# Kernel optimization log

Measured on AMD Instinct MI355X. Metric: run time of the kernel, lower is better.

## Reference

```python
import jax, jax.numpy as jnp
import numpy as np

N, K, F = 262144, 256, 128
LAMB = 1.0
EPS = 1e-16


def setup_inputs() -> dict:
    key = jax.random.key(0)
    kx, = jax.random.split(key, 1)
    x = jax.random.normal(kx, (N, F), dtype=jnp.float32)
    # Faithful SVD-orthonormal init of cluster centers (num_clusters > feature_size branch)
    rng = np.random.RandomState(0)
    m_np = rng.rand(K, F)
    m_np = m_np.T                      # (F, K) since K > F
    _, _, vh = np.linalg.svd(m_np, full_matrices=False)  # vh: (F, K)
    m_np = vh[:K].T                    # (K, F), orthonormal columns
    m = jnp.asarray(m_np, dtype=jnp.float32)
    s1 = jnp.ones((K,), dtype=jnp.float32)
    s2 = jnp.ones((K,), dtype=jnp.float32)
    return {"x": x, "m": m, "s1": s1, "s2": s2}


def _p_all(x, m, s):
    # x: (N,F), m: (K,F), s: (K,) -> p: (N,K)
    # squared distances via gram expansion (single GEMM instead of per-sample loop)
    d2 = (jnp.sum(x * x, axis=1, keepdims=True)
          + jnp.sum(m * m, axis=1)[None, :]
          - 2.0 * (x @ m.T))
    d2 = jnp.maximum(d2, 0.0)
    logits = -d2 / (s * s)[None, :]
    return jax.nn.softmax(logits, axis=-1)


def _entropy(p):
    # shannon entropy with the original's clamping of p into (0,1)
    p = jnp.clip(p, EPS, 1.0 - EPS)
    return -jnp.sum(p * jnp.log(p), axis=-1)


def reference(x, m, s1, s2):
    # F.normalize(x): L2-normalize rows with eps=1e-12
    xn = x / jnp.maximum(jnp.linalg.norm(x, axis=1, keepdims=True), 1e-12)
    p = _p_all(xn, m, s1)              # (N,K)
    intra = jnp.mean(_entropy(p))      # scalar
    # inter: entropy of the assignment of the mean center against all centers
    xm = jnp.mean(m, axis=0)           # (F,)
    d = jnp.linalg.norm(xm[None, :] - m, axis=1)  # (K,)
    pi = jax.nn.softmax(-((d / s2) ** 2))
    inter = _entropy(pi)
    total = intra - LAMB * inter
    return (total, intra, inter)
```

## Files before the change

kernel.cpp:

```cpp
#include <hip/hip_runtime.h>
#include <hip/hip_bf16.h>


#define N_ROWS 262144

typedef __attribute__((ext_vector_type(8))) short bf16x8;
typedef __attribute__((ext_vector_type(4))) float f32x4;
typedef __attribute__((ext_vector_type(4))) unsigned short u16x4;

__device__ __forceinline__ unsigned short bf16_rne(float x) {
    unsigned int u = __float_as_uint(x);
    u += 0x7FFFu + ((u >> 16) & 1u);
    return (unsigned short)(u >> 16);
}
__device__ __forceinline__ float bf16f(unsigned short h) {
    return __uint_as_float(((unsigned int)h) << 16);
}

__global__ __launch_bounds__(256) void prep(
    const float* __restrict__ m, const float* __restrict__ s1,
    unsigned short* __restrict__ mhi_g, float* __restrict__ mn2_g,
    float* __restrict__ invs_g)
{
    const int t    = threadIdx.x;
    const int lane = t & 63;
    const int k    = blockIdx.x * 8 + (t >> 5);
    const int f4   = t & 31;
    float4 v = reinterpret_cast<const float4*>(m)[k * 32 + f4];
    float pn = v.x*v.x + v.y*v.y + v.z*v.z + v.w*v.w;
    #pragma unroll
    for (int msk = 1; msk <= 16; msk <<= 1) pn += __shfl_xor(pn, msk);
    if ((lane & 31) == 0) {
        mn2_g[k] = pn;
        float sv = s1[k];
        invs_g[k] = 1.0f / (sv * sv);
    }
    const int f0 = f4 << 2;
    const int c = k >> 4, n = k & 15, s = f0 >> 5, blk = (f0 >> 3) & 3, i0 = f0 & 7;
    const int elem = ((c * 4 + s) * 64 + blk * 16 + n) * 8 + i0;
    float xs[4] = {v.x, v.y, v.z, v.w};
    u16x4 hh;
    #pragma unroll
    for (int q = 0; q < 4; ++q) hh[q] = bf16_rne(xs[q]);
    *(u16x4*)(mhi_g + elem) = hh;
}

__global__ __launch_bounds__(512, 4) void fused_main(
    const float* __restrict__ x, const unsigned short* __restrict__ mhi_g,
    const float* __restrict__ mn2_g, const float* __restrict__ invs_g,
    float* __restrict__ blocksum)
{
    extern __shared__ char smem[];
    unsigned short* mhi = (unsigned short*)smem;
    float* mn2  = (float*)(smem + 65536);
    float* invs = (float*)(smem + 65536 + 1024);
    float* entw = (float*)(smem + 65536 + 2048);

    const int tid  = threadIdx.x;
    const int lane = tid & 63;
    const int w    = tid >> 6;
    const int rw   = lane & 15;
    const int blkl = lane >> 4;

    {
        const uint4* s4 = (const uint4*)mhi_g;
        uint4* d4 = (uint4*)mhi;
        #pragma unroll
        for (int it = 0; it < 8; ++it) d4[tid + it * 512] = s4[tid + it * 512];
        if (tid < 256) { mn2[tid] = mn2_g[tid]; invs[tid] = invs_g[tid]; }
    }
    __syncthreads();

    const int rbase = blockIdx.x * 128 + w * 16;
    const float* xrow = x + (size_t)(rbase + rw) * 128 + blkl * 8;

    f32x4 acc[16];
    #pragma unroll
    for (int c = 0; c < 16; ++c) acc[c] = f32x4{0.f, 0.f, 0.f, 0.f};

    float n2 = 0.0f;
    float4 u = *(const float4*)(xrow);
    float4 v = *(const float4*)(xrow + 4);

    #pragma unroll
    for (int s = 0; s < 4; ++s) {
        bf16x8 ahi, alo;
        {
            float xs[8] = {u.x, u.y, u.z, u.w, v.x, v.y, v.z, v.w};
            #pragma unroll
            for (int q = 0; q < 8; ++q) {
                n2 += xs[q] * xs[q];
                unsigned short h = bf16_rne(xs[q]);
                float r = xs[q] - bf16f(h);
                ahi[q] = (short)h;
                alo[q] = (short)bf16_rne(r);
            }
        }
        if (s < 3) {
            u = *(const float4*)(xrow + (s + 1) * 32);
            v = *(const float4*)(xrow + (s + 1) * 32 + 4);
        }
        #pragma unroll
        for (int c = 0; c < 16; ++c) {
            bf16x8 bh = *(const bf16x8*)(mhi + ((c * 4 + s) * 64 + lane) * 8);
            acc[c] = __builtin_amdgcn_mfma_f32_16x16x32_bf16(alo, bh, acc[c], 0, 0, 0);
            acc[c] = __builtin_amdgcn_mfma_f32_16x16x32_bf16(ahi, bh, acc[c], 0, 0, 0);
        }
    }

    n2 += __shfl_xor(n2, 16);
    n2 += __shfl_xor(n2, 32);
    float a2 = 2.0f / fmaxf(sqrtf(n2), 1e-12f);
    float arow[4];
    #pragma unroll
    for (int reg = 0; reg < 4; ++reg)
        arow[reg] = __shfl(a2, blkl * 4 + reg);

    float bkv[16], isv[16];
    #pragma unroll
    for (int c = 0; c < 16; ++c) {
        int col = c * 16 + rw;
        bkv[c] = 1.0f + mn2[col];
        isv[c] = invs[col];
    }

    float ent = 0.0f;
    #pragma unroll
    for (int reg = 0; reg < 4; ++reg) {
        float S = 0.f, T = 0.f;
        #pragma unroll
        for (int c = 0; c < 16; ++c) {
            float l = fminf(arow[reg] * acc[c][reg] - bkv[c], 0.0f) * isv[c];
            float e = __expf(l);
            S += e;
            T += l * e;
        }
        #pragma unroll
        for (int msk = 1; msk <= 8; msk <<= 1) {
            S += __shfl_xor(S, msk);
            T += __shfl_xor(T, msk);
        }
        if (rw == 0) ent += __logf(S) - T / S;
    }
    ent += __shfl_xor(ent, 16);
    ent += __shfl_xor(ent, 32);
    if (lane == 0) entw[w] = ent;
    __syncthreads();
    if (tid == 0) {
        float b = 0.f;
        #pragma unroll
        for (int i = 0; i < 8; ++i) b += entw[i];
        blocksum[blockIdx.x] = b;
    }
}

__global__ __launch_bounds__(256) void finalize(
    const float* __restrict__ blocksum, const float* __restrict__ m,
    const float* __restrict__ s2, float* __restrict__ out)
{
    __shared__ float xmp[256];
    __shared__ float xm[128];
    __shared__ double dred[4];
    __shared__ float redM[4], redS[4], redT[4];
    const int tid = threadIdx.x;
    const int lane = tid & 63;
    const int w = tid >> 6;

    double ds = 0.0;
    #pragma unroll
    for (int j = 0; j < 8; ++j) ds += (double)blocksum[tid + 256 * j];
    #pragma unroll
    for (int msk = 1; msk <= 32; msk <<= 1) ds += __shfl_xor(ds, msk);
    if (lane == 0) dred[w] = ds;

    {
        const int f = tid & 127, half = tid >> 7;
        const float* mp = m + (size_t)half * 128 * 128 + f;
        float cs = 0.f;
        #pragma unroll 8
        for (int k = 0; k < 128; ++k) cs += mp[(size_t)k * 128];
        xmp[tid] = cs;
    }
    __syncthreads();
    if (tid < 128) xm[tid] = (xmp[tid] + xmp[tid + 128]) * (1.0f / 256.0f);
    __syncthreads();

    float d2 = 0.f;
    {
        const float4* mr = (const float4*)(m + (size_t)tid * 128);
        const float4* xv4 = (const float4*)xm;
        #pragma unroll 8
        for (int j = 0; j < 32; ++j) {
            float4 mv = mr[j], xv = xv4[j];
            float dx = xv.x - mv.x, dy = xv.y - mv.y,
                  dz = xv.z - mv.z, dw = xv.w - mv.w;
            d2 += dx*dx + dy*dy + dz*dz + dw*dw;
        }
    }
    float dd = sqrtf(d2);
    float r = dd / s2[tid];
    float lg = -(r * r);

    float mx = lg;
    #pragma unroll
    for (int msk = 1; msk <= 32; msk <<= 1) mx = fmaxf(mx, __shfl_xor(mx, msk));
    if (lane == 0) redM[w] = mx;
    __syncthreads();
    float bmx = fmaxf(fmaxf(redM[0], redM[1]), fmaxf(redM[2], redM[3]));
    float d = lg - bmx;
    float e = __expf(d);
    float S = e, T = d * e;
    #pragma unroll
    for (int msk = 1; msk <= 32; msk <<= 1) {
        S += __shfl_xor(S, msk);
        T += __shfl_xor(T, msk);
    }
    if (lane == 0) { redS[w] = S; redT[w] = T; }
    __syncthreads();
    if (tid == 0) {
        float Sa = redS[0] + redS[1] + redS[2] + redS[3];
        float Ta = redT[0] + redT[1] + redT[2] + redT[3];
        float inter = __logf(Sa) - Ta / Sa;
        double intra_d = dred[0] + dred[1] + dred[2] + dred[3];
        float intra = (float)(intra_d / (double)N_ROWS);
        out[0] = intra - inter;
        out[1] = intra;
        out[2] = inter;
    }
}

extern "C" void kernel_launch(void* const* d_in, const int* in_sizes, int n_in,
                              void* d_out, int out_size, void* d_ws, size_t ws_size,
                              hipStream_t stream) {
    const float* x  = (const float*)d_in[0];
    const float* m  = (const float*)d_in[1];
    const float* s1 = (const float*)d_in[2];
    const float* s2 = (const float*)d_in[3];
    float* out = (float*)d_out;

    char* ws = (char*)d_ws;
    unsigned short* mhi_g = (unsigned short*)ws;
    float* mn2_g  = (float*)(ws + 65536);
    float* invs_g = (float*)(ws + 65536 + 1024);
    float* blocksum = (float*)(ws + 65536 + 2048);

    const size_t shbytes = 65536 + 2048 + 32;
    static bool attr_set = false;
    if (!attr_set) {
        (void)hipFuncSetAttribute((const void*)fused_main,
                                  hipFuncAttributeMaxDynamicSharedMemorySize,
                                  (int)shbytes);
        attr_set = true;
    }

    prep<<<dim3(32), dim3(256), 0, stream>>>(m, s1, mhi_g, mn2_g, invs_g);
    fused_main<<<dim3(2048), dim3(512), shbytes, stream>>>(x, mhi_g, mn2_g, invs_g, blocksum);
    finalize<<<dim3(1), dim3(256), 0, stream>>>(blocksum, m, s2, out);
}
```

Baseline: 225.9 us.

## Hold centroid matrix in registers and loop each wave over many row tiles

The main kernel now runs as a persistent-style grid of 256 blocks. Each wave keeps the whole bf16 centroid matrix in registers (64 bf16x8 vectors) and processes 16 tiles of 16 rows, prefetching the next tile's x while computing the current one. This removes the per-block LDS copy of the centroids, the per-fragment LDS reads and the block-level sync. The cost is very high register pressure at one block of 256 threads per CU, so there is little occupancy left to hide latency. The finalize kernel is widened to 1024 threads, drops its max-reduction, and sums per-wave partials.

```diff
diff --git a/kernel.cpp b/kernel.cpp
--- a/kernel.cpp
+++ b/kernel.cpp
@@ -45,171 +45,158 @@
     *(u16x4*)(mhi_g + elem) = hh;
 }
 
-__global__ __launch_bounds__(512, 4) void fused_main(
+__global__ __launch_bounds__(256, 1) void fused_main(
     const float* __restrict__ x, const unsigned short* __restrict__ mhi_g,
     const float* __restrict__ mn2_g, const float* __restrict__ invs_g,
-    float* __restrict__ blocksum)
+    float* __restrict__ wavesum)
 {
-    extern __shared__ char smem[];
-    unsigned short* mhi = (unsigned short*)smem;
-    float* mn2  = (float*)(smem + 65536);
-    float* invs = (float*)(smem + 65536 + 1024);
-    float* entw = (float*)(smem + 65536 + 2048);
-
     const int tid  = threadIdx.x;
     const int lane = tid & 63;
     const int w    = tid >> 6;
     const int rw   = lane & 15;
     const int blkl = lane >> 4;
-
-    {
-        const uint4* s4 = (const uint4*)mhi_g;
-        uint4* d4 = (uint4*)mhi;
-        #pragma unroll
-        for (int it = 0; it < 8; ++it) d4[tid + it * 512] = s4[tid + it * 512];
-        if (tid < 256) { mn2[tid] = mn2_g[tid]; invs[tid] = invs_g[tid]; }
-    }
-    __syncthreads();
-
-    const int rbase = blockIdx.x * 128 + w * 16;
-    const float* xrow = x + (size_t)(rbase + rw) * 128 + blkl * 8;
-
-    f32x4 acc[16];
-    #pragma unroll
-    for (int c = 0; c < 16; ++c) acc[c] = f32x4{0.f, 0.f, 0.f, 0.f};
-
-    float n2 = 0.0f;
-    float4 u = *(const float4*)(xrow);
-    float4 v = *(const float4*)(xrow + 4);
-
+    const int gw   = blockIdx.x * 4 + w;
+
+    bf16x8 B[64];
+    #pragma unroll
+    for (int j = 0; j < 64; ++j)
+        B[j] = *(const bf16x8*)(mhi_g + (j * 64 + lane) * 8);
+
+    float bkv[16], isv[16];
+    #pragma unroll
+    for (int c = 0; c < 16; ++c) {
+        bkv[c] = 1.0f + mn2_g[c * 16 + rw];
+        isv[c] = invs_g[c * 16 + rw];
+    }
+
+    const float* xbase = x + (size_t)(gw * 256 + rw) * 128 + blkl * 8;
+
+    float4 px[8];
     #pragma unroll
     for (int s = 0; s < 4; ++s) {
-        bf16x8 ahi, alo;
-        {
-            float xs[8] = {u.x, u.y, u.z, u.w, v.x, v.y, v.z, v.w};
+        px[2*s]   = *(const float4*)(xbase + s * 32);
+        px[2*s+1] = *(const float4*)(xbase + s * 32 + 4);
+    }
+
+    float ent = 0.0f;
+
+    for (int t = 0; t < 16; ++t) {
+        bf16x8 ah[4], al[4];
+        float n2 = 0.0f;
+        #pragma unroll
+        for (int s = 0; s < 4; ++s) {
+            float xs[8] = {px[2*s].x, px[2*s].y, px[2*s].z, px[2*s].w,
+                           px[2*s+1].x, px[2*s+1].y, px[2*s+1].z, px[2*s+1].w};
             #pragma unroll
             for (int q = 0; q < 8; ++q) {
                 n2 += xs[q] * xs[q];
                 unsigned short h = bf16_rne(xs[q]);
                 float r = xs[q] - bf16f(h);
-                ahi[q] = (short)h;
-                alo[q] = (short)bf16_rne(r);
-            }
-        }
-        if (s < 3) {
-            u = *(const float4*)(xrow + (s + 1) * 32);
-            v = *(const float4*)(xrow + (s + 1) * 32 + 4);
-        }
-        #pragma unroll
-        for (int c = 0; c < 16; ++c) {
-            bf16x8 bh = *(const bf16x8*)(mhi + ((c * 4 + s) * 64 + lane) * 8);
-            acc[c] = __builtin_amdgcn_mfma_f32_16x16x32_bf16(alo, bh, acc[c], 0, 0, 0);
-            acc[c] = __builtin_amdgcn_mfma_f32_16x16x32_bf16(ahi, bh, acc[c], 0, 0, 0);
-        }
-    }
-
-    n2 += __shfl_xor(n2, 16);
-    n2 += __shfl_xor(n2, 32);
-    float a2 = 2.0f / fmaxf(sqrtf(n2), 1e-12f);
-    float arow[4];
-    #pragma unroll
-    for (int reg = 0; reg < 4; ++reg)
-        arow[reg] = __shfl(a2, blkl * 4 + reg);
-
-    float bkv[16], isv[16];
-    #pragma unroll
-    for (int c = 0; c < 16; ++c) {
-        int col = c * 16 + rw;
-        bkv[c] = 1.0f + mn2[col];
-        isv[c] = invs[col];
-    }
-
-    float ent = 0.0f;
-    #pragma unroll
-    for (int reg = 0; reg < 4; ++reg) {
-        float S = 0.f, T = 0.f;
-        #pragma unroll
-        for (int c = 0; c < 16; ++c) {
-            float l = fminf(arow[reg] * acc[c][reg] - bkv[c], 0.0f) * isv[c];
-            float e = __expf(l);
-            S += e;
-            T += l * e;
-        }
-        #pragma unroll
-        for (int msk = 1; msk <= 8; msk <<= 1) {
-            S += __shfl_xor(S, msk);
-            T += __shfl_xor(T, msk);
-        }
-        if (rw == 0) ent += __logf(S) - T / S;
-    }
+                ah[s][q] = (short)h;
+                al[s][q] = (short)bf16_rne(r);
+            }
+        }
+        if (t != 15) {
+            const float* p = xbase + (size_t)(t + 1) * 16 * 128;
+            #pragma unroll
+            for (int s = 0; s < 4; ++s) {
+                px[2*s]   = *(const float4*)(p + s * 32);
+                px[2*s+1] = *(const float4*)(p + s * 32 + 4);
+            }
+        }
+        f32x4 acc[16];
+        #pragma unroll
+        for (int c = 0; c < 16; ++c) acc[c] = f32x4{0.f, 0.f, 0.f, 0.f};
+        #pragma unroll
+        for (int s = 0; s < 4; ++s) {
+            #pragma unroll
+            for (int c = 0; c < 16; ++c) {
+                acc[c] = __builtin_amdgcn_mfma_f32_16x16x32_bf16(al[s], B[c*4+s], acc[c], 0, 0, 0);
+                acc[c] = __builtin_amdgcn_mfma_f32_16x16x32_bf16(ah[s], B[c*4+s], acc[c], 0, 0, 0);
+            }
+        }
+        n2 += __shfl_xor(n2, 16);
+        n2 += __shfl_xor(n2, 32);
+        float a2 = 2.0f / fmaxf(sqrtf(n2), 1e-12f);
+        #pragma unroll
+        for (int reg = 0; reg < 4; ++reg) {
+            float ar = __shfl(a2, blkl * 4 + reg);
+            float S = 0.f, T = 0.f;
+            #pragma unroll
+            for (int c = 0; c < 16; ++c) {
+                float l = fminf(ar * acc[c][reg] - bkv[c], 0.0f) * isv[c];
+                float e = __expf(l);
+                S += e;
+                T += l * e;
+            }
+            #pragma unroll
+            for (int msk = 1; msk <= 8; msk <<= 1) {
+                S += __shfl_xor(S, msk);
+                T += __shfl_xor(T, msk);
+            }
+            if (rw == 0) ent += __logf(S) - T / S;
+        }
+    }
+
     ent += __shfl_xor(ent, 16);
     ent += __shfl_xor(ent, 32);
-    if (lane == 0) entw[w] = ent;
-    __syncthreads();
-    if (tid == 0) {
-        float b = 0.f;
-        #pragma unroll
-        for (int i = 0; i < 8; ++i) b += entw[i];
-        blocksum[blockIdx.x] = b;
-    }
-}
-
-__global__ __launch_bounds__(256) void finalize(
-    const float* __restrict__ blocksum, const float* __restrict__ m,
+    if (lane == 0) wavesum[gw] = ent;
+}
+
+__global__ __launch_bounds__(1024) void finalize(
+    const float* __restrict__ wavesum, const float* __restrict__ m,
     const float* __restrict__ s2, float* __restrict__ out)
 {
-    __shared__ float xmp[256];
+    __shared__ float xmp[8][128];
     __shared__ float xm[128];
-    __shared__ double dred[4];
-    __shared__ float redM[4], redS[4], redT[4];
-    const int tid = threadIdx.x;
+    __shared__ double dred[16];
+    __shared__ float redS[16], redT[16];
+    const int tid  = threadIdx.x;
     const int lane = tid & 63;
-    const int w = tid >> 6;
-
-    double ds = 0.0;
-    #pragma unroll
-    for (int j = 0; j < 8; ++j) ds += (double)blocksum[tid + 256 * j];
+    const int w    = tid >> 6;
+
+    double ds = (double)wavesum[tid];
     #pragma unroll
     for (int msk = 1; msk <= 32; msk <<= 1) ds += __shfl_xor(ds, msk);
     if (lane == 0) dred[w] = ds;
 
     {
-        const int f = tid & 127, half = tid >> 7;
-        const float* mp = m + (size_t)half * 128 * 128 + f;
+        const int f = tid & 127, g = tid >> 7;
+        const float* mp = m + (size_t)g * 32 * 128 + f;
         float cs = 0.f;
         #pragma unroll 8
-        for (int k = 0; k < 128; ++k) cs += mp[(size_t)k * 128];
-        xmp[tid] = cs;
+        for (int k = 0; k < 32; ++k) cs += mp[(size_t)k * 128];
+        xmp[g][f] = cs;
     }
     __syncthreads();
-    if (tid < 128) xm[tid] = (xmp[tid] + xmp[tid + 128]) * (1.0f / 256.0f);
+    if (tid < 128) {
+        float s = 0.f;
+        #pragma unroll
+        for (int g = 0; g < 8; ++g) s += xmp[g][tid];
+        xm[tid] = s * (1.0f / 256.0f);
+    }
     __syncthreads();
 
+    const int k = tid >> 2, q = tid & 3;
     float d2 = 0.f;
     {
-        const float4* mr = (const float4*)(m + (size_t)tid * 128);
-        const float4* xv4 = (const float4*)xm;
-        #pragma unroll 8
-        for (int j = 0; j < 32; ++j) {
+        const float4* mr  = (const float4*)(m + (size_t)k * 128) + q * 8;
+        const float4* xv4 = (const float4*)xm + q * 8;
+        #pragma unroll
+        for (int j = 0; j < 8; ++j) {
             float4 mv = mr[j], xv = xv4[j];
             float dx = xv.x - mv.x, dy = xv.y - mv.y,
                   dz = xv.z - mv.z, dw = xv.w - mv.w;
             d2 += dx*dx + dy*dy + dz*dz + dw*dw;
         }
     }
-    float dd = sqrtf(d2);
-    float r = dd / s2[tid];
-    float lg = -(r * r);
-
-    float mx = lg;
-    #pragma unroll
-    for (int msk = 1; msk <= 32; msk <<= 1) mx = fmaxf(mx, __shfl_xor(mx, msk));
-    if (lane == 0) redM[w] = mx;
-    __syncthreads();
-    float bmx = fmaxf(fmaxf(redM[0], redM[1]), fmaxf(redM[2], redM[3]));
-    float d = lg - bmx;
-    float e = __expf(d);
-    float S = e, T = d * e;
+    d2 += __shfl_xor(d2, 1);
+    d2 += __shfl_xor(d2, 2);
+    float sv = s2[k];
+    float rr = sqrtf(d2) / sv;
+    float lg = -(rr * rr);
+    float e  = (q == 0) ? __expf(lg) : 0.f;
+    float S = e, T = (q == 0) ? lg * e : 0.f;
     #pragma unroll
     for (int msk = 1; msk <= 32; msk <<= 1) {
         S += __shfl_xor(S, msk);
@@ -218,10 +205,13 @@
     if (lane == 0) { redS[w] = S; redT[w] = T; }
     __syncthreads();
     if (tid == 0) {
-        float Sa = redS[0] + redS[1] + redS[2] + redS[3];
-        float Ta = redT[0] + redT[1] + redT[2] + redT[3];
+        float Sa = 0.f, Ta = 0.f;
+        double intra_d = 0.0;
+        #pragma unroll
+        for (int i = 0; i < 16; ++i) {
+            Sa += redS[i]; Ta += redT[i]; intra_d += dred[i];
+        }
         float inter = __logf(Sa) - Ta / Sa;
-        double intra_d = dred[0] + dred[1] + dred[2] + dred[3];
         float intra = (float)(intra_d / (double)N_ROWS);
         out[0] = intra - inter;
         out[1] = intra;
@@ -240,20 +230,11 @@
 
     char* ws = (char*)d_ws;
     unsigned short* mhi_g = (unsigned short*)ws;
-    float* mn2_g  = (float*)(ws + 65536);
-    float* invs_g = (float*)(ws + 65536 + 1024);
-    float* blocksum = (float*)(ws + 65536 + 2048);
-
-    const size_t shbytes = 65536 + 2048 + 32;
-    static bool attr_set = false;
-    if (!attr_set) {
-        (void)hipFuncSetAttribute((const void*)fused_main,
-                                  hipFuncAttributeMaxDynamicSharedMemorySize,
-                                  (int)shbytes);
-        attr_set = true;
-    }
+    float* mn2_g   = (float*)(ws + 65536);
+    float* invs_g  = (float*)(ws + 65536 + 1024);
+    float* wavesum = (float*)(ws + 65536 + 2048);
 
     prep<<<dim3(32), dim3(256), 0, stream>>>(m, s1, mhi_g, mn2_g, invs_g);
-    fused_main<<<dim3(2048), dim3(512), shbytes, stream>>>(x, mhi_g, mn2_g, invs_g, blocksum);
-    finalize<<<dim3(1), dim3(256), 0, stream>>>(blocksum, m, s2, out);
-}
+    fused_main<<<dim3(256), dim3(256), 0, stream>>>(x, mhi_g, mn2_g, invs_g, wavesum);
+    finalize<<<dim3(1), dim3(1024), 0, stream>>>(wavesum, m, s2, out);
+}
```

After: 249.0 us. +10.2%, slower.
